# Kernel tuning notes

Hardware: AMD Instinct MI355X
Metric: run time of the kernel (lower is better)

## Reference

```python
import jax, jax.numpy as jnp
import numpy as np

NUM_LAYERS = 2
D_MODEL = 64
D_INNER = 128   # expand * d_model
D_STATE = 128   # min(2*input_size, 256)
DT_RANK = 4     # ceil(d_model / 16)
D_CONV = 4
HIDDEN = 64


def _causal_dwconv(x, w, b):
    # x: [B, L, C], w: [C, K], b: [C]  -- causal depthwise conv (left pad K-1)
    K = w.shape[1]
    L = x.shape[1]
    xp = jnp.pad(x, ((0, 0), (K - 1, 0), (0, 0)))
    y = sum(xp[:, k:k + L, :] * w[:, k][None, None, :] for k in range(K))
    return y + b


def _selective_scan(u, delta, A, B, C, Dp):
    # u, delta: [b,L,d]; A: [d,n]; B, C: [b,L,n]; Dp: [d]
    dA = jnp.exp(jnp.einsum('bld,dn->lbdn', delta, A))          # [L,b,d,n]
    dBu = jnp.einsum('bld,bln,bld->lbdn', delta, B, u)           # [L,b,d,n]
    Ct = jnp.swapaxes(C, 0, 1)                                   # [L,b,n]

    def step(h, inp):
        dA_t, dBu_t, C_t = inp
        h = dA_t * h + dBu_t                                     # [b,d,n]
        y = jnp.einsum('bdn,bn->bd', h, C_t)
        return h, y

    h0 = jnp.zeros(dA.shape[1:], dA.dtype)
    _, ys = jax.lax.scan(step, h0, (dA, dBu, Ct))                # ys: [L,b,d]
    return jnp.swapaxes(ys, 0, 1) + u * Dp


def _mamba_layer(x, in_w, conv_w, conv_b, xproj_w, dt_w, dt_b, A_log, Dp, out_w):
    xz = x @ in_w.T                                              # [B,L,2*d_inner]
    xi, z = jnp.split(xz, 2, axis=-1)
    xi = jax.nn.silu(_causal_dwconv(xi, conv_w, conv_b))
    xdbl = xi @ xproj_w.T                                        # [B,L,dt_rank+2*d_state]
    delta = jax.nn.softplus(xdbl[..., :DT_RANK] @ dt_w.T + dt_b)
    Bm = xdbl[..., DT_RANK:DT_RANK + D_STATE]
    Cm = xdbl[..., DT_RANK + D_STATE:]
    A = -jnp.exp(A_log)
    y = _selective_scan(xi, delta, A, Bm, Cm, Dp)
    y = y * jax.nn.silu(z)
    return y @ out_w.T


def setup_inputs() -> dict:
    key = jax.random.key(0)
    ks = jax.random.split(key, 10)
    B, L = 4, 1024
    s = 0.05
    x = jax.random.normal(ks[0], (B, L, D_MODEL), dtype=jnp.float32)
    in_proj_w = jax.random.normal(ks[1], (NUM_LAYERS, 2 * D_INNER, D_MODEL)) * s
    conv_w = jax.random.normal(ks[2], (NUM_LAYERS, D_INNER, D_CONV)) * 0.2
    conv_b = jax.random.normal(ks[3], (NUM_LAYERS, D_INNER)) * 0.02
    x_proj_w = jax.random.normal(ks[4], (NUM_LAYERS, DT_RANK + 2 * D_STATE, D_INNER)) * s
    dt_w = jax.random.normal(ks[5], (NUM_LAYERS, D_INNER, DT_RANK)) * 0.1
    dt_b = jnp.full((NUM_LAYERS, D_INNER), -4.6, dtype=jnp.float32)  # softplus -> ~0.01
    # S4D-real init: A_log = log(1..d_state)
    A_log = jnp.log(jnp.broadcast_to(
        jnp.arange(1, D_STATE + 1, dtype=jnp.float32), (NUM_LAYERS, D_INNER, D_STATE)))
    D = jnp.ones((NUM_LAYERS, D_INNER), dtype=jnp.float32)
    out_proj_w = jax.random.normal(ks[6], (NUM_LAYERS, D_MODEL, D_INNER)) * s
    fc_w = jax.random.normal(ks[7], (HIDDEN, D_MODEL)) * s
    fc_b = jax.random.normal(ks[8], (HIDDEN,)) * 0.02
    return {"x": x, "in_proj_w": in_proj_w, "conv_w": conv_w, "conv_b": conv_b,
            "x_proj_w": x_proj_w, "dt_w": dt_w, "dt_b": dt_b, "A_log": A_log,
            "D": D, "out_proj_w": out_proj_w, "fc_w": fc_w, "fc_b": fc_b}


def reference(x, in_proj_w, conv_w, conv_b, x_proj_w, dt_w, dt_b, A_log, D, out_proj_w, fc_w, fc_b):
    h = x
    for l in range(NUM_LAYERS):
        h = _mamba_layer(h, in_proj_w[l], conv_w[l], conv_b[l], x_proj_w[l],
                         dt_w[l], dt_b[l], A_log[l], D[l], out_proj_w[l])
    return h @ fc_w.T + fc_b
```

## Files before the change

### kernel.cpp

```cpp
#include <hip/hip_runtime.h>
#include <hip/hip_bf16.h>
#include <hip/hip_cooperative_groups.h>

namespace cg = cooperative_groups;

#define BB 4
#define LL 1024
#define DM 64
#define DI 128
#define DS 128
#define DTR 4
#define KC 4
#define RT 8
#define GRP 8
#define CS 128
#define NC 8
#define L2E 1.44269504f

#define XWT_OFF   0
#define INWT_OFF  65536
#define OWT_OFF   98304
#define CWT_OFF   114688
#define CB_OFF    115712
#define DTWT_OFF  115968
#define DTB_OFF   116992
#define XWDT_OFF  117248

__device__ __forceinline__ float bf2f(__hip_bfloat16 v) { return __bfloat162float(v); }
__device__ __forceinline__ float silu_f(float x) { return x / (1.f + __expf(-x)); }

__device__ __forceinline__ float ldf(const void* p, long i, unsigned bf) {
    return bf ? __bfloat162float(((const __hip_bfloat16*)p)[i]) : ((const float*)p)[i];
}

__device__ __forceinline__ void fma4(float4& acc, float s, const float4 w) {
    acc.x = fmaf(s, w.x, acc.x); acc.y = fmaf(s, w.y, acc.y);
    acc.z = fmaf(s, w.z, acc.z); acc.w = fmaf(s, w.w, acc.w);
}

__device__ __forceinline__ void probe_flags(const void* dtb, const void* fcw,
                                            unsigned& bfe, unsigned& bfw) {
    unsigned w = *(const unsigned*)dtb;
    bfe = (w == 0xC093C093u) ? 1u : 0u;
    const unsigned* p = (const unsigned*)fcw;
    int cnt = 0;
    for (int i = 0; i < 32; ++i) {
        unsigned m = p[i] & 0x7FFFu;
        if (m >= 0x3000u && m < 0x4200u) cnt++;
    }
    bfw = (cnt >= 28) ? 1u : 0u;
}

__global__ __launch_bounds__(256) void k_prep(
        const void* __restrict__ inw, const void* __restrict__ xw,
        const void* __restrict__ ow, const void* __restrict__ cw,
        const void* __restrict__ cb, const void* __restrict__ dtw,
        const void* __restrict__ dtb, const void* __restrict__ fcw,
        unsigned* __restrict__ flags, float* __restrict__ WT) {
    unsigned bfe, bfw;
    probe_flags(dtb, fcw, bfe, bfw);
    int bid = blockIdx.x, tid = threadIdx.x;
    if (bid < 28) {
        const void* src; long soff; int srcK; float* dst; int dstN; int n0, k0;
        if (bid < 16) {
            int l = bid >> 3, kt = (bid >> 2) & 1, nt = bid & 3;
            src = xw; srcK = 128; soff = (long)l * 260 * 128 + 4 * 128;
            n0 = nt * 64; k0 = kt * 64; dst = WT + XWT_OFF + l * 32768; dstN = 256;
        } else if (bid < 24) {
            int b2 = bid - 16, l = b2 >> 2, nt = b2 & 3;
            src = inw; srcK = 64; soff = (long)l * 256 * 64;
            n0 = nt * 64; k0 = 0; dst = WT + INWT_OFF + l * 16384; dstN = 256;
        } else {
            int b2 = bid - 24, l = b2 >> 1, kt = b2 & 1;
            src = ow; srcK = 128; soff = (long)l * 64 * 128;
            n0 = 0; k0 = kt * 64; dst = WT + OWT_OFF + l * 8192; dstN = 64;
        }
        __shared__ float tile[64 * 65];
        for (int i = tid; i < 4096; i += 256) {
            int ln = i >> 6, lk = i & 63;
            tile[ln * 65 + lk] = ldf(src, soff + (long)(n0 + ln) * srcK + k0 + lk, bfw);
        }
        __syncthreads();
        for (int i = tid; i < 4096; i += 256) {
            int lk = i >> 6, ln = i & 63;
            dst[(long)(k0 + lk) * dstN + n0 + ln] = tile[ln * 65 + lk];
        }
    } else {
        if (tid == 0) { flags[0] = bfe; flags[1] = bfw; flags[2] = bfe & bfw; }
        for (int j = tid; j < 1024; j += 256) {
            int l = j >> 9, t = (j >> 7) & 3, d = j & 127;
            WT[CWT_OFF + j] = ldf(cw, (long)l * 512 + d * 4 + t, bfw);
        }
        for (int j = tid; j < 256; j += 256) WT[CB_OFF + j] = ldf(cb, j, bfw);
        for (int j = tid; j < 1024; j += 256) {
            int l = j >> 9, r = (j >> 7) & 3, d = j & 127;
            WT[DTWT_OFF + j] = ldf(dtw, (long)l * 512 + d * 4 + r, bfw);
        }
        for (int j = tid; j < 256; j += 256) WT[DTB_OFF + j] = ldf(dtb, j, bfe);
        for (int j = tid; j < 1024; j += 256) {
            int l = j >> 9, rem = j & 511;
            WT[XWDT_OFF + j] = ldf(xw, (long)l * 260 * 128 + rem, bfw);
        }
    }
}

__global__ __launch_bounds__(256) void k_inproj(
        const void* __restrict__ xin, int xin_probe,
        const float* __restrict__ wt, const unsigned* __restrict__ flags,
        float* __restrict__ xzx, float* __restrict__ sz) {
    unsigned bfx = xin_probe ? flags[0] : 0u;
    int row0 = blockIdx.x * RT;
    int tid = threadIdx.x, lane = tid & 63, g = tid >> 6;
    __shared__ float act[RT * DM];
    for (int i = tid; i < RT * DM; i += 256)
        act[i] = ldf(xin, (long)(row0 + (i >> 6)) * DM + (i & 63), bfx);
    __syncthreads();
    const float4* wt4 = (const float4*)wt;
    float4 acc[2];
    acc[0] = make_float4(0.f, 0.f, 0.f, 0.f);
    acc[1] = make_float4(0.f, 0.f, 0.f, 0.f);
#pragma unroll 8
    for (int k4 = 0; k4 < DM / 4; ++k4) {
        float4 w0 = wt4[(k4 * 4 + 0) * 64 + lane];
        float4 w1 = wt4[(k4 * 4 + 1) * 64 + lane];
        float4 w2 = wt4[(k4 * 4 + 2) * 64 + lane];
        float4 w3 = wt4[(k4 * 4 + 3) * 64 + lane];
#pragma unroll
        for (int r = 0; r < 2; ++r) {
            float4 av = *(const float4*)&act[(g * 2 + r) * DM + k4 * 4];
            fma4(acc[r], av.x, w0); fma4(acc[r], av.y, w1);
            fma4(acc[r], av.z, w2); fma4(acc[r], av.w, w3);
        }
    }
    int n0 = lane * 4;
#pragma unroll
    for (int r = 0; r < 2; ++r) {
        int row = row0 + g * 2 + r;
        if (n0 < DI) {
            *(float4*)&xzx[(size_t)row * DI + n0] = acc[r];
        } else {
            float4 v;
            v.x = silu_f(acc[r].x); v.y = silu_f(acc[r].y);
            v.z = silu_f(acc[r].z); v.w = silu_f(acc[r].w);
            *(float4*)&sz[(size_t)row * DI + (n0 - DI)] = v;
        }
    }
}

__global__ __launch_bounds__(256) void k_xproj(
        const float* __restrict__ xzx,
        const float* __restrict__ cwT, const float* __restrict__ cbF,
        const float* __restrict__ xwT, const float* __restrict__ xwdtF,
        const float* __restrict__ dtwT, const float* __restrict__ dtbF,
        float* __restrict__ xiw, float* __restrict__ dlt,
        float* __restrict__ Bm, float* __restrict__ Cm) {
    int row0 = blockIdx.x * RT;
    int b = row0 >> 10, l0 = row0 & (LL - 1);
    int tid = threadIdx.x, lane = tid & 63, g = tid >> 6;
    __shared__ float xc[(RT + KC - 1) * DI];
    __shared__ float act[RT * DI];
    __shared__ float dtp[RT * DTR];
    for (int i = tid; i < (RT + KC - 1) * DI; i += 256) {
        int r = (i >> 7) - (KC - 1);
        int l = l0 + r;
        xc[i] = (l >= 0) ? xzx[((size_t)b * LL + l) * DI + (i & 127)] : 0.f;
    }
    __syncthreads();
    for (int i = tid; i < RT * DI; i += 256) {
        int r = i >> 7, d = i & 127;
        float a = cbF[d];
#pragma unroll
        for (int t = 0; t < KC; ++t) a = fmaf(xc[(r + t) * DI + d], cwT[t * DI + d], a);
        float v = silu_f(a);
        act[i] = v;
        xiw[(size_t)(row0 + r) * DI + d] = v;
    }
    __syncthreads();
    const float4* wt4 = (const float4*)xwT;
    float4 acc[2];
    acc[0] = make_float4(0.f, 0.f, 0.f, 0.f);
    acc[1] = make_float4(0.f, 0.f, 0.f, 0.f);
#pragma unroll 8
    for (int k4 = 0; k4 < DI / 4; ++k4) {
        float4 w0 = wt4[(k4 * 4 + 0) * 64 + lane];
        float4 w1 = wt4[(k4 * 4 + 1) * 64 + lane];
        float4 w2 = wt4[(k4 * 4 + 2) * 64 + lane];
        float4 w3 = wt4[(k4 * 4 + 3) * 64 + lane];
#pragma unroll
        for (int r = 0; r < 2; ++r) {
            float4 av = *(const float4*)&act[(g * 2 + r) * DI + k4 * 4];
            fma4(acc[r], av.x, w0); fma4(acc[r], av.y, w1);
            fma4(acc[r], av.z, w2); fma4(acc[r], av.w, w3);
        }
    }
    int n0 = lane * 4;
#pragma unroll
    for (int r = 0; r < 2; ++r) {
        int row = row0 + g * 2 + r;
        if (n0 < DS) *(float4*)&Bm[(size_t)row * DS + n0] = acc[r];
        else         *(float4*)&Cm[(size_t)row * DS + (n0 - DS)] = acc[r];
    }
    if (tid < RT * DTR) {
        int r = tid >> 2, i = tid & 3;
        float a = 0.f;
#pragma unroll
        for (int k4 = 0; k4 < DI / 4; ++k4) {
            float4 av = *(const float4*)&act[r * DI + k4 * 4];
            float4 wv = *(const float4*)&xwdtF[i * DI + k4 * 4];
            a = fmaf(av.x, wv.x, a); a = fmaf(av.y, wv.y, a);
            a = fmaf(av.z, wv.z, a); a = fmaf(av.w, wv.w, a);
        }
        dtp[tid] = a;
    }
    __syncthreads();
    if (tid < DI) {
        float dw0 = dtwT[0 * DI + tid], dw1 = dtwT[1 * DI + tid];
        float dw2 = dtwT[2 * DI + tid], dw3 = dtwT[3 * DI + tid];
        float bv = dtbF[tid];
#pragma unroll
        for (int r = 0; r < RT; ++r) {
            float a = bv;
            a = fmaf(dtp[r * 4 + 0], dw0, a);
            a = fmaf(dtp[r * 4 + 1], dw1, a);
            a = fmaf(dtp[r * 4 + 2], dw2, a);
            a = fmaf(dtp[r * 4 + 3], dw3, a);
            dlt[(size_t)(row0 + r) * DI + tid] = (a > 20.f) ? a : log1pf(__expf(a));
        }
    }
}

__global__ __launch_bounds__(256) void k_scanF(
        const float* __restrict__ dlt, const float* __restrict__ xiw,
        const float* __restrict__ Bm, const float* __restrict__ Cm,
        const void* __restrict__ Alog, long aoff,
        const void* __restrict__ Dp, long doff,
        const unsigned* __restrict__ flags,
        float* __restrict__ hend, float* __restrict__ S,
        float* __restrict__ y) {
    __shared__ float dsh[CS * 4];
    __shared__ float dush[CS * 4];
    __shared__ float cdsh[CS * 4];
    __shared__ float ysh[CS * 4];
    __shared__ float Wred[4 * 520];
    int gid = blockIdx.x;
    int dg = gid / (BB * NC);
    int bc = gid % (BB * NC);
    int b = bc / NC, c = bc % NC;
    int d0 = dg * 4;
    int tid = threadIdx.x;
    int w = tid >> 6, t = tid & 63;
    int d = d0 + w;
    int c0 = c * CS;
    unsigned bfe = flags[0];
    float A0 = -L2E * __expf(ldf(Alog, aoff + (long)d * DS + 2 * t, bfe));
    float A1 = -L2E * __expf(ldf(Alog, aoff + (long)d * DS + 2 * t + 1, bfe));
    for (int i = tid; i < CS * 4; i += 256) {
        size_t src = ((size_t)b * LL + c0 + (i >> 2)) * DI + d0 + (i & 3);
        float dl = dlt[src];
        float ul = xiw[src];
        dsh[i] = dl;
        dush[i] = dl * ul;
        ysh[i] = ul * ldf(Dp, doff + d0 + (i & 3), bfe);
    }
    __syncthreads();
    {
        float a = dsh[t * 4 + w];
        float bb2 = dsh[(64 + t) * 4 + w];
#pragma unroll
        for (int off = 1; off < 64; off <<= 1) {
            float n = __shfl(a, t - off, 64);
            if (t >= off) a += n;
        }
        float T1 = __shfl(a, 63, 64);
#pragma unroll
        for (int off = 1; off < 64; off <<= 1) {
            float n = __shfl(bb2, t - off, 64);
            if (t >= off) bb2 += n;
        }
        bb2 += T1;
        cdsh[t * 4 + w] = a;
        cdsh[(64 + t) * 4 + w] = bb2;
    }
    const float2* Bg = (const float2*)(Bm + ((size_t)b * LL + c0) * DS) + t;
    const float2* Cg = (const float2*)(Cm + ((size_t)b * LL + c0) * DS) + t;
    float* Wl = Wred + w * 520;
    int rbase = (t >> 3) * 65 + (t & 7) * 8;
    float h0 = 0.f, h1v = 0.f;
    for (int li = 0; li < CS; li += GRP) {
        float dl[GRP], du[GRP], ea0[GRP], ea1[GRP], cv[GRP];
        float2 Bv[GRP], Cv[GRP];
#pragma unroll
        for (int s = 0; s < GRP; ++s) {
            dl[s] = dsh[(li + s) * 4 + w];
            du[s] = dush[(li + s) * 4 + w];
            Bv[s] = Bg[(size_t)(li + s) * (DS / 2)];
            Cv[s] = Cg[(size_t)(li + s) * (DS / 2)];
        }
#pragma unroll
        for (int s = 0; s < GRP; ++s) {
            ea0[s] = exp2f(dl[s] * A0);
            ea1[s] = exp2f(dl[s] * A1);
        }
#pragma unroll
        for (int s = 0; s < GRP; ++s) {
            h0  = fmaf(ea0[s], h0,  du[s] * Bv[s].x);
            h1v = fmaf(ea1[s], h1v, du[s] * Bv[s].y);
            cv[s] = fmaf(h0, Cv[s].x, h1v * Cv[s].y);
        }
#pragma unroll
        for (int s = 0; s < GRP; ++s) Wl[s * 65 + t] = cv[s];
        float pt = 0.f;
#pragma unroll
        for (int j = 0; j < 8; ++j) pt += Wl[rbase + j];
        pt += __shfl_xor(pt, 1, 64);
        pt += __shfl_xor(pt, 2, 64);
        pt += __shfl_xor(pt, 4, 64);
        if ((t & 7) == 0) {
            int l = li + (t >> 3);
            ysh[l * 4 + w] += pt;
        }
    }
    if (c < NC - 1) {
        size_t hbase = (((size_t)b * DI + d) * NC + c) * DS;
        ((float2*)(hend + hbase))[t] = make_float2(h0, h1v);
        if (t == 0) S[((size_t)b * DI + d) * NC + c] = cdsh[127 * 4 + w];
    }
    __threadfence();
    cg::this_grid().sync();
    if (c > 0) {
        float hi0 = 0.f, hi1 = 0.f;
        const float2* hep = (const float2*)(hend + (((size_t)b * DI + d) * NC) * DS);
        const float* Sp = S + ((size_t)b * DI + d) * NC;
        for (int cc = 0; cc < c; ++cc) {
            float2 he = hep[(size_t)cc * (DS / 2) + t];
            float s = Sp[cc];
            hi0 = fmaf(exp2f(A0 * s), hi0, he.x);
            hi1 = fmaf(exp2f(A1 * s), hi1, he.y);
        }
        for (int li = 0; li < CS; li += GRP) {
            float cd[GRP], ea0[GRP], ea1[GRP], cv[GRP];
            float2 Cv[GRP];
#pragma unroll
            for (int s = 0; s < GRP; ++s) {
                cd[s] = cdsh[(li + s) * 4 + w];
                Cv[s] = Cg[(size_t)(li + s) * (DS / 2)];
            }
#pragma unroll
            for (int s = 0; s < GRP; ++s) {
                ea0[s] = exp2f(cd[s] * A0);
                ea1[s] = exp2f(cd[s] * A1);
            }
#pragma unroll
            for (int s = 0; s < GRP; ++s)
                cv[s] = fmaf(hi0 * ea0[s], Cv[s].x, hi1 * ea1[s] * Cv[s].y);
#pragma unroll
            for (int s = 0; s < GRP; ++s) Wl[s * 65 + t] = cv[s];
            float pt = 0.f;
#pragma unroll
            for (int j = 0; j < 8; ++j) pt += Wl[rbase + j];
            pt += __shfl_xor(pt, 1, 64);
            pt += __shfl_xor(pt, 2, 64);
            pt += __shfl_xor(pt, 4, 64);
            if ((t & 7) == 0) {
                int l = li + (t >> 3);
                ysh[l * 4 + w] += pt;
            }
        }
    }
    __syncthreads();
    for (int i = tid; i < CS * 4; i += 256)
        y[((size_t)b * LL + c0 + (i >> 2)) * DI + d0 + (i & 3)] = ysh[i];
}

__global__ __launch_bounds__(256) void k_scanA(
        const float* __restrict__ dlt, const float* __restrict__ xiw,
        const float* __restrict__ Bm,
        const void* __restrict__ Alog, long aoff,
        const unsigned* __restrict__ flags,
        float* __restrict__ hend, float* __restrict__ S) {
    __shared__ float dsh[CS * 4];
    __shared__ float ush[CS * 4];
    int gid = blockIdx.x;
    int dg = gid / (BB * NC);
    int bc = gid % (BB * NC);
    int b = bc / NC, c = bc % NC;
    int d0 = dg * 4;
    int tid = threadIdx.x;
    int w = tid >> 6, t = tid & 63;
    int d = d0 + w;
    int c0 = c * CS;
    unsigned bfe = flags[0];
    float A0 = -L2E * __expf(ldf(Alog, aoff + (long)d * DS + 2 * t, bfe));
    float A1 = -L2E * __expf(ldf(Alog, aoff + (long)d * DS + 2 * t + 1, bfe));
    for (int i = tid; i < CS * 4; i += 256) {
        size_t src = ((size_t)b * LL + c0 + (i >> 2)) * DI + d0 + (i & 3);
        dsh[i] = dlt[src];
        ush[i] = xiw[src];
    }
    __syncthreads();
    const float2* Bg = (const float2*)(Bm + ((size_t)b * LL + c0) * DS) + t;
    float h0 = 0.f, h1v = 0.f, sumd = 0.f;
    for (int li = 0; li < CS; li += GRP) {
        float dl[GRP], ul[GRP], ea0[GRP], ea1[GRP];
        float2 Bv[GRP];
#pragma unroll
        for (int s = 0; s < GRP; ++s) {
            dl[s] = dsh[(li + s) * 4 + w];
            ul[s] = ush[(li + s) * 4 + w];
            Bv[s] = Bg[(size_t)(li + s) * (DS / 2)];
        }
#pragma unroll
        for (int s = 0; s < GRP; ++s) {
            ea0[s] = exp2f(dl[s] * A0);
            ea1[s] = exp2f(dl[s] * A1);
        }
#pragma unroll
        for (int s = 0; s < GRP; ++s) {
            float db = dl[s] * ul[s];
            h0  = fmaf(ea0[s], h0,  db * Bv[s].x);
            h1v = fmaf(ea1[s], h1v, db * Bv[s].y);
            sumd += dl[s];
        }
    }
    size_t hbase = (((size_t)b * DI + d) * NC + c) * DS;
    ((float2*)(hend + hbase))[t] = make_float2(h0, h1v);
    if (t == 0) S[((size_t)b * DI + d) * NC + c] = sumd;
}

__global__ __launch_bounds__(256) void k_scanC(
        const float* __restrict__ dlt, const float* __restrict__ xiw,
        const float* __restrict__ Bm, const float* __restrict__ Cm,
        const void* __restrict__ Alog, long aoff,
        const void* __restrict__ Dp, long doff,
        const unsigned* __restrict__ flags,
        const float* __restrict__ hend, const float* __restrict__ S,
        float* __restrict__ y) {
    __shared__ float dsh[CS * 4];
    __shared__ float ush[CS * 4];
    __shared__ float ysh[CS * 4];
    __shared__ float Wred[4 * 520];
    int gid = blockIdx.x;
    int dg = gid / (BB * NC);
    int bc = gid % (BB * NC);
    int b = bc / NC, c = bc % NC;
    int d0 = dg * 4;
    int tid = threadIdx.x;
    int w = tid >> 6, t = tid & 63;
    int d = d0 + w;
    int c0 = c * CS;
    unsigned bfe = flags[0];
    float A0 = -L2E * __expf(ldf(Alog, aoff + (long)d * DS + 2 * t, bfe));
    float A1 = -L2E * __expf(ldf(Alog, aoff + (long)d * DS + 2 * t + 1, bfe));
    float Dv = ldf(Dp, doff + d, bfe);
    for (int i = tid; i < CS * 4; i += 256) {
        size_t src = ((size_t)b * LL + c0 + (i >> 2)) * DI + d0 + (i & 3);
        dsh[i] = dlt[src];
        ush[i] = xiw[src];
    }
    __syncthreads();
    float h0 = 0.f, h1v = 0.f;
    const float2* hep = (const float2*)(hend + (((size_t)b * DI + d) * NC) * DS);
    const float* Sp = S + ((size_t)b * DI + d) * NC;
    for (int cc = 0; cc < c; ++cc) {
        float2 he = hep[(size_t)cc * (DS / 2) + t];
        float s = Sp[cc];
        h0  = fmaf(exp2f(A0 * s), h0,  he.x);
        h1v = fmaf(exp2f(A1 * s), h1v, he.y);
    }
    const float2* Bg = (const float2*)(Bm + ((size_t)b * LL + c0) * DS) + t;
    const float2* Cg = (const float2*)(Cm + ((size_t)b * LL + c0) * DS) + t;
    float* Wl = Wred + w * 520;
    int rbase = (t >> 3) * 65 + (t & 7) * 8;
    for (int li = 0; li < CS; li += GRP) {
        float dl[GRP], ul[GRP], ea0[GRP], ea1[GRP], cv[GRP];
        float2 Bv[GRP], Cv[GRP];
#pragma unroll
        for (int s = 0; s < GRP; ++s) {
            dl[s] = dsh[(li + s) * 4 + w];
            ul[s] = ush[(li + s) * 4 + w];
            Bv[s] = Bg[(size_t)(li + s) * (DS / 2)];
            Cv[s] = Cg[(size_t)(li + s) * (DS / 2)];
        }
#pragma unroll
        for (int s = 0; s < GRP; ++s) {
            ea0[s] = exp2f(dl[s] * A0);
            ea1[s] = exp2f(dl[s] * A1);
        }
#pragma unroll
        for (int s = 0; s < GRP; ++s) {
            float db = dl[s] * ul[s];
            h0  = fmaf(ea0[s], h0,  db * Bv[s].x);
            h1v = fmaf(ea1[s], h1v, db * Bv[s].y);
            cv[s] = fmaf(h0, Cv[s].x, h1v * Cv[s].y);
        }
#pragma unroll
        for (int s = 0; s < GRP; ++s) Wl[s * 65 + t] = cv[s];
        float pt = 0.f;
#pragma unroll
        for (int j = 0; j < 8; ++j) pt += Wl[rbase + j];
        pt += __shfl_xor(pt, 1, 64);
        pt += __shfl_xor(pt, 2, 64);
        pt += __shfl_xor(pt, 4, 64);
        if ((t & 7) == 0) {
            int l = li + (t >> 3);
            ysh[l * 4 + w] = pt + ush[l * 4 + w] * Dv;
        }
    }
    __syncthreads();
    for (int i = tid; i < CS * 4; i += 256)
        y[((size_t)b * LL + c0 + (i >> 2)) * DI + d0 + (i & 3)] = ysh[i];
}

__global__ __launch_bounds__(256) void k_out(
        const float* __restrict__ y, const float* __restrict__ sz,
        const float* __restrict__ owT, float* __restrict__ hout) {
    int row0 = blockIdx.x * RT;
    int tid = threadIdx.x, n = tid & 63, g = tid >> 6;
    __shared__ float act[RT * DI];
    for (int i = tid; i < RT * DI; i += 256) {
        size_t idx = (size_t)(row0 + (i >> 7)) * DI + (i & 127);
        act[i] = y[idx] * sz[idx];
    }
    __syncthreads();
    float acc[2] = {0.f, 0.f};
#pragma unroll 8
    for (int k4 = 0; k4 < DI / 4; ++k4) {
        float w0 = owT[(k4 * 4 + 0) * DM + n];
        float w1 = owT[(k4 * 4 + 1) * DM + n];
        float w2 = owT[(k4 * 4 + 2) * DM + n];
        float w3 = owT[(k4 * 4 + 3) * DM + n];
#pragma unroll
        for (int r = 0; r < 2; ++r) {
            float4 av = *(const float4*)&act[(g * 2 + r) * DI + k4 * 4];
            acc[r] = fmaf(av.x, w0, acc[r]); acc[r] = fmaf(av.y, w1, acc[r]);
            acc[r] = fmaf(av.z, w2, acc[r]); acc[r] = fmaf(av.w, w3, acc[r]);
        }
    }
#pragma unroll
    for (int r = 0; r < 2; ++r)
        hout[(size_t)(row0 + g * 2 + r) * DM + n] = acc[r];
}

__global__ __launch_bounds__(256) void k_fc(
        const float* __restrict__ h, const void* __restrict__ fw,
        const void* __restrict__ fb, const unsigned* __restrict__ flags,
        void* __restrict__ out) {
    unsigned bfw = flags[1], obf = flags[2];
    int row0 = blockIdx.x * RT;
    int tid = threadIdx.x, n = tid & 63, g = tid >> 6;
    __shared__ float wsh[DM * 65];
    __shared__ float act[RT * DM];
    for (int i = tid; i < DM * DM; i += 256) {
        int nn = i >> 6, k = i & 63;
        wsh[k * 65 + nn] = ldf(fw, i, bfw);
    }
    for (int i = tid; i < RT * DM; i += 256)
        act[i] = h[(size_t)(row0 + (i >> 6)) * DM + (i & 63)];
    __syncthreads();
    float bv = ldf(fb, n, bfw);
    float acc[2] = {bv, bv};
#pragma unroll 8
    for (int k4 = 0; k4 < DM / 4; ++k4) {
        float w0 = wsh[(k4 * 4 + 0) * 65 + n];
        float w1 = wsh[(k4 * 4 + 1) * 65 + n];
        float w2 = wsh[(k4 * 4 + 2) * 65 + n];
        float w3 = wsh[(k4 * 4 + 3) * 65 + n];
#pragma unroll
        for (int r = 0; r < 2; ++r) {
            float4 av = *(const float4*)&act[(g * 2 + r) * DM + k4 * 4];
            acc[r] = fmaf(av.x, w0, acc[r]); acc[r] = fmaf(av.y, w1, acc[r]);
            acc[r] = fmaf(av.z, w2, acc[r]); acc[r] = fmaf(av.w, w3, acc[r]);
        }
    }
#pragma unroll
    for (int r = 0; r < 2; ++r) {
        size_t idx = (size_t)(row0 + g * 2 + r) * DM + n;
        if (obf) ((__hip_bfloat16*)out)[idx] = __float2bfloat16(acc[r]);
        else     ((float*)out)[idx] = acc[r];
    }
}

extern "C" void kernel_launch(void* const* d_in, const int* in_sizes, int n_in,
                              void* d_out, int out_size, void* d_ws, size_t ws_size,
                              hipStream_t stream) {
    const void* x    = d_in[0];
    const void* inw  = d_in[1];
    const void* cw   = d_in[2];
    const void* cb   = d_in[3];
    const void* xw   = d_in[4];
    const void* dtw  = d_in[5];
    const void* dtb  = d_in[6];
    const void* Alog = d_in[7];
    const void* Dp   = d_in[8];
    const void* ow   = d_in[9];
    const void* fcw  = d_in[10];
    const void* fcb  = d_in[11];

    const size_t NBL = (size_t)BB * LL;
    const int GB = (int)(NBL / RT);
    unsigned* flags = (unsigned*)d_ws;
    float* base = (float*)d_ws + 64;
    float* h1   = base;
    float* sz   = h1 + 262144;
    float* xiw  = sz + 524288;
    float* dlt  = xiw + 524288;
    float* Bmw  = dlt + 524288;
    float* Cmw  = Bmw + 524288;
    float* yw   = Cmw + 524288;
    float* hend = yw + 524288;
    float* S    = hend + 524288;
    float* xzx  = yw;
    float* WT   = (float*)d_out;

    int nb = 0;
    hipOccupancyMaxActiveBlocksPerMultiprocessor(&nb, k_scanF, 256, 0);
    const bool coop = (nb >= 4);

    k_prep<<<29, 256, 0, stream>>>(inw, xw, ow, cw, cb, dtw, dtb, fcw, flags, WT);

    for (int l = 0; l < 2; ++l) {
        const void* xin = (l == 0) ? x : (const void*)h1;
        int xmode = (l == 0) ? 1 : 0;
        k_inproj<<<GB, 256, 0, stream>>>(xin, xmode, WT + INWT_OFF + l * 16384, flags, xzx, sz);
        k_xproj<<<GB, 256, 0, stream>>>(xzx,
                                        WT + CWT_OFF + l * 512, WT + CB_OFF + l * 128,
                                        WT + XWT_OFF + l * 32768, WT + XWDT_OFF + l * 512,
                                        WT + DTWT_OFF + l * 512, WT + DTB_OFF + l * 128,
                                        xiw, dlt, Bmw, Cmw);
        long ao = (long)l * DI * DS;
        long dof = (long)l * DI;
        if (coop) {
            const float* dlt_c = dlt; const float* xiw_c = xiw;
            const float* Bm_c = Bmw; const float* Cm_c = Cmw;
            const unsigned* fl_c = flags;
            void* params[] = {
                (void*)&dlt_c, (void*)&xiw_c, (void*)&Bm_c, (void*)&Cm_c,
                (void*)&Alog, (void*)&ao, (void*)&Dp, (void*)&dof,
                (void*)&fl_c, (void*)&hend, (void*)&S, (void*)&yw
            };
            hipLaunchCooperativeKernel((const void*)k_scanF, dim3(32 * BB * NC),
                                       dim3(256), params, 0, stream);
        } else {
            k_scanA<<<32 * BB * NC, 256, 0, stream>>>(dlt, xiw, Bmw, Alog, ao, flags, hend, S);
            k_scanC<<<32 * BB * NC, 256, 0, stream>>>(dlt, xiw, Bmw, Cmw, Alog, ao,
                                                      Dp, dof, flags, hend, S, yw);
        }
        k_out<<<GB, 256, 0, stream>>>(yw, sz, WT + OWT_OFF + l * 8192, h1);
    }
    k_fc<<<GB, 256, 0, stream>>>(h1, fcw, fcb, flags, d_out);
}
```

Before: 295.4 us.

## Halve scan chunk size to double chunk-parallel blocks and reorder carry combine

Splits the sequence into 16 chunks of 64 instead of 8 of 128, which doubles the number of scan blocks and halves the serial per-chunk work. The cumulative-delta prefix now needs only a single 64-lane wavefront scan. The inter-chunk carry is accumulated in reverse with a running decay sum, so the two sequential FMA chains are replaced by independent terms. The cost is more carry passes and a larger end-state buffer. The cooperative path now requires 8 resident blocks per CU, so it may fall back to the non-cooperative path.

```diff
diff --git a/kernel.cpp b/kernel.cpp
--- a/kernel.cpp
+++ b/kernel.cpp
@@ -13,8 +13,8 @@
 #define KC 4
 #define RT 8
 #define GRP 8
-#define CS 128
-#define NC 8
+#define CS 64
+#define NC 16
 #define L2E 1.44269504f
 
 #define XWT_OFF   0
@@ -265,21 +265,12 @@
     __syncthreads();
     {
         float a = dsh[t * 4 + w];
-        float bb2 = dsh[(64 + t) * 4 + w];
 #pragma unroll
         for (int off = 1; off < 64; off <<= 1) {
             float n = __shfl(a, t - off, 64);
             if (t >= off) a += n;
         }
-        float T1 = __shfl(a, 63, 64);
-#pragma unroll
-        for (int off = 1; off < 64; off <<= 1) {
-            float n = __shfl(bb2, t - off, 64);
-            if (t >= off) bb2 += n;
-        }
-        bb2 += T1;
         cdsh[t * 4 + w] = a;
-        cdsh[(64 + t) * 4 + w] = bb2;
     }
     const float2* Bg = (const float2*)(Bm + ((size_t)b * LL + c0) * DS) + t;
     const float2* Cg = (const float2*)(Cm + ((size_t)b * LL + c0) * DS) + t;
@@ -323,19 +314,19 @@
     if (c < NC - 1) {
         size_t hbase = (((size_t)b * DI + d) * NC + c) * DS;
         ((float2*)(hend + hbase))[t] = make_float2(h0, h1v);
-        if (t == 0) S[((size_t)b * DI + d) * NC + c] = cdsh[127 * 4 + w];
+        if (t == 0) S[((size_t)b * DI + d) * NC + c] = cdsh[(CS - 1) * 4 + w];
     }
     __threadfence();
     cg::this_grid().sync();
     if (c > 0) {
-        float hi0 = 0.f, hi1 = 0.f;
+        float hi0 = 0.f, hi1 = 0.f, ssum = 0.f;
         const float2* hep = (const float2*)(hend + (((size_t)b * DI + d) * NC) * DS);
         const float* Sp = S + ((size_t)b * DI + d) * NC;
-        for (int cc = 0; cc < c; ++cc) {
+        for (int cc = c - 1; cc >= 0; --cc) {
             float2 he = hep[(size_t)cc * (DS / 2) + t];
-            float s = Sp[cc];
-            hi0 = fmaf(exp2f(A0 * s), hi0, he.x);
-            hi1 = fmaf(exp2f(A1 * s), hi1, he.y);
+            hi0 = fmaf(exp2f(A0 * ssum), he.x, hi0);
+            hi1 = fmaf(exp2f(A1 * ssum), he.y, hi1);
+            ssum += Sp[cc];
         }
         for (int li = 0; li < CS; li += GRP) {
             float cd[GRP], ea0[GRP], ea1[GRP], cv[GRP];
@@ -458,14 +449,14 @@
         ush[i] = xiw[src];
     }
     __syncthreads();
-    float h0 = 0.f, h1v = 0.f;
+    float h0 = 0.f, h1v = 0.f, ssum = 0.f;
     const float2* hep = (const float2*)(hend + (((size_t)b * DI + d) * NC) * DS);
     const float* Sp = S + ((size_t)b * DI + d) * NC;
-    for (int cc = 0; cc < c; ++cc) {
+    for (int cc = c - 1; cc >= 0; --cc) {
         float2 he = hep[(size_t)cc * (DS / 2) + t];
-        float s = Sp[cc];
-        h0  = fmaf(exp2f(A0 * s), h0,  he.x);
-        h1v = fmaf(exp2f(A1 * s), h1v, he.y);
+        h0  = fmaf(exp2f(A0 * ssum), he.x, h0);
+        h1v = fmaf(exp2f(A1 * ssum), he.y, h1v);
+        ssum += Sp[cc];
     }
     const float2* Bg = (const float2*)(Bm + ((size_t)b * LL + c0) * DS) + t;
     const float2* Cg = (const float2*)(Cm + ((size_t)b * LL + c0) * DS) + t;
@@ -608,13 +599,13 @@
     float* Cmw  = Bmw + 524288;
     float* yw   = Cmw + 524288;
     float* hend = yw + 524288;
-    float* S    = hend + 524288;
+    float* S    = hend + 1048576;
     float* xzx  = yw;
     float* WT   = (float*)d_out;
 
     int nb = 0;
     hipOccupancyMaxActiveBlocksPerMultiprocessor(&nb, k_scanF, 256, 0);
-    const bool coop = (nb >= 4);
+    const bool coop = (nb >= 8);
 
     k_prep<<<29, 256, 0, stream>>>(inw, xw, ow, cw, cb, dtw, dtb, fcw, flags, WT);
 
```

Measured after the change: 299.0 us. No clear change (+1.2%).
